# Kernel tuning notes

Hardware: AMD Instinct MI355X
Metric: run time of the kernel (lower is better)

Reference implementation:

```python
import jax, jax.numpy as jnp
import numpy as np

B = 4096        # batch size (graphs)
NPB = 64        # nodes per graph
G = 8           # max_groups; first G nodes of each graph are group super-nodes
D = 128         # node_dim
GD = 128        # global_dim
H = 64          # hidden_dim
NEG = jnp.float32(-1e9)


def setup_inputs() -> dict:
    key = jax.random.key(0)
    k = jax.random.split(key, 5)
    node_features = jax.random.normal(k[0], (B * NPB, D), dtype=jnp.float32)
    global_features = jax.random.normal(k[1], (B, GD), dtype=jnp.float32)
    # nodes sorted by graph: graph b owns rows [b*NPB, (b+1)*NPB)
    batch = jnp.repeat(jnp.arange(B, dtype=jnp.int64), NPB)
    local_id = jnp.tile(jnp.arange(NPB), B)
    group_mask_nodes = local_id < G            # exactly G group nodes per graph, in order
    dock_mask = jax.random.bernoulli(k[2], 0.7, (B, G, G))
    W1 = jax.random.normal(k[3], (GD + 2 * D, H), dtype=jnp.float32) * 0.05
    b1 = jnp.zeros((H,), dtype=jnp.float32)
    W2 = jax.random.normal(k[4], (H, 1), dtype=jnp.float32) * 0.05
    b2 = jnp.zeros((1,), dtype=jnp.float32)
    return {
        "node_features": node_features,
        "global_features": global_features,
        "group_mask_nodes": group_mask_nodes,
        "batch": batch,
        "dock_mask": dock_mask,
        "W1": W1, "b1": b1, "W2": W2, "b2": b2,
    }


def reference(node_features, global_features, group_mask_nodes, batch, dock_mask, W1, b1, W2, b2):
    bsz = global_features.shape[0]
    g = dock_mask.shape[1]
    d = node_features.shape[-1]
    # Gather group super-nodes. Rows are sorted by graph with exactly g group
    # nodes per graph, so a static-size nonzero reshapes to [B, G, D] preserving
    # the row order the torch loop relies on.
    idx = jnp.nonzero(group_mask_nodes, size=bsz * g)[0]
    group_nodes = node_features[idx].reshape(bsz, g, d)           # [B,G,D]
    # Build all (i,j) pair features: [global_b, g_i, g_j] -> [B,G,G,GD+2D]
    glob = jnp.broadcast_to(global_features[:, None, None, :], (bsz, g, g, global_features.shape[-1]))
    gi = jnp.broadcast_to(group_nodes[:, :, None, :], (bsz, g, g, d))
    gj = jnp.broadcast_to(group_nodes[:, None, :, :], (bsz, g, g, d))
    inp = jnp.concatenate([glob, gi, gj], axis=-1)
    # Tiny 2-layer MLP scorer, fully batched over all pairs.
    h = jax.nn.relu(jnp.einsum('bijf,fh->bijh', inp, W1) + b1)
    scores = jnp.einsum('bijh,ho->bijo', h, W2)[..., 0] + b2[0]   # [B,G,G]
    offdiag = ~jnp.eye(g, dtype=bool)
    logits = jnp.where(offdiag[None, :, :], scores, NEG)
    logits = jnp.where(dock_mask, logits, NEG)
    return logits.reshape(bsz, g * g)
```

## Files before the change

### kernel.cpp

```cpp
#include <hip/hip_runtime.h>
#include <hip/hip_bf16.h>

#define NEGV (-1e9f)

typedef __attribute__((ext_vector_type(8))) short short8;
typedef __attribute__((ext_vector_type(4))) float f32x4;

#define MFMA16(a, b, c) __builtin_amdgcn_mfma_f32_16x16x32_bf16(a, b, c, 0, 0, 0)

__device__ __forceinline__ unsigned short f2bf(float x) {
    union { __hip_bfloat16 h; unsigned short u; } c;
    c.h = __float2bfloat16(x);
    return c.u;
}

__device__ __forceinline__ short8 pack2(f32x4 a, f32x4 b) {
    short8 r;
    r[0] = (short)f2bf(a[0]); r[1] = (short)f2bf(a[1]);
    r[2] = (short)f2bf(a[2]); r[3] = (short)f2bf(a[3]);
    r[4] = (short)f2bf(b[0]); r[5] = (short)f2bf(b[1]);
    r[6] = (short)f2bf(b[2]); r[7] = (short)f2bf(b[3]);
    return r;
}

__device__ __forceinline__ void gather_mat(const float* __restrict__ Wp, int lg, short8* out4) {
    float tv[32];
#pragma unroll
    for (int x = 0; x < 32; ++x) {
        const int kt = x >> 3, i = x & 7;
        tv[x] = Wp[(kt * 32 + lg * 8 + i) * 64];
    }
#pragma unroll
    for (int kt = 0; kt < 4; ++kt) {
        short8 r;
#pragma unroll
        for (int i = 0; i < 8; ++i) r[i] = (short)f2bf(tv[kt * 8 + i]);
        out4[kt] = r;
    }
}

__global__ __launch_bounds__(256, 4) void dock_main(
    const float* __restrict__ nodes,
    const float* __restrict__ glob,
    const int*   __restrict__ dock,
    const float* __restrict__ W1,
    const float* __restrict__ b1,
    const float* __restrict__ b2,
    const float* __restrict__ W2,
    float* __restrict__ out)
{
    __shared__ __align__(16) unsigned char gA[32 * 256];
    __shared__ __align__(16) unsigned char gGl[16 * 256];
    __shared__ float sPQ[32][132];
    __shared__ float sA[4][68];

    const int t    = threadIdx.x;
    const int lane = t & 63;
    const int w    = __builtin_amdgcn_readfirstlane(t >> 6);
    const int b0   = blockIdx.x * 4;
    const int lr   = lane & 15, lg = lane >> 4;

    const int sr = t >> 3, sc0 = (t & 7) * 16;
    const f32x4* ns4 = (const f32x4*)(nodes + ((size_t)(b0 + (sr >> 3)) * 64 + (sr & 7)) * 128 + sc0);
    const f32x4 nf0 = ns4[0], nf1 = ns4[1], nf2 = ns4[2], nf3 = ns4[3];

    const int gr = t >> 4, gc0 = (t & 15) * 8;
    f32x4 gf0 = (f32x4)0.f, gf1 = (f32x4)0.f;
    if (gr < 4) {
        const f32x4* gs4 = (const f32x4*)(glob + (size_t)(b0 + gr) * 128 + gc0);
        gf0 = gs4[0]; gf1 = gs4[1];
    }
    const int idx   = (b0 + w) * 64 + lane;
    const int dmask = dock[idx];
    const float b1v = b1[w * 16 + lr];
    const float b2v = b2[0];

    const int n0 = w * 32 + lr;
    const int n1 = n0 + 16;
    const float* Wp0 = (n0 < 64) ? W1 + 128 * 64 + n0 : W1 + 256 * 64 + (n0 - 64);
    const float* Wp1 = (n1 < 64) ? W1 + 128 * 64 + n1 : W1 + 256 * 64 + (n1 - 64);
    const float* Wpg = W1 + (w * 16 + lr);

    short8 wf[12];
    gather_mat(Wp0, lg, wf);
    gather_mat(Wp1, lg, wf + 4);
    gather_mat(Wpg, lg, wf + 8);

    {
        const int u0 = sc0 >> 3;
        *(short8*)(gA + sr * 256 + ((u0 ^ (sr & 7)) << 4))       = pack2(nf0, nf1);
        *(short8*)(gA + sr * 256 + (((u0 + 1) ^ (sr & 7)) << 4)) = pack2(nf2, nf3);
        short8 gv = (short8)0;
        if (gr < 4) gv = pack2(gf0, gf1);
        *(short8*)(gGl + gr * 256 + (((gc0 >> 3) ^ (gr & 7)) << 4)) = gv;
    }
    __syncthreads();

    f32x4 acc00 = (f32x4)0.f, acc01 = (f32x4)0.f;
    f32x4 acc10 = (f32x4)0.f, acc11 = (f32x4)0.f;
    f32x4 accA  = (f32x4)0.f;
#pragma unroll
    for (int kt = 0; kt < 4; ++kt) {
        const int sw = ((kt * 4 + lg) ^ (lr & 7)) << 4;
        short8 aG0 = *(const short8*)(gA + lr * 256 + sw);
        short8 aG1 = *(const short8*)(gA + (16 + lr) * 256 + sw);
        short8 aGl = *(const short8*)(gGl + lr * 256 + sw);
        acc00 = MFMA16(aG0, wf[kt],     acc00);
        acc01 = MFMA16(aG0, wf[4 + kt], acc01);
        acc10 = MFMA16(aG1, wf[kt],     acc10);
        acc11 = MFMA16(aG1, wf[4 + kt], acc11);
        accA  = MFMA16(aGl, wf[8 + kt], accA);
    }

#pragma unroll
    for (int r = 0; r < 4; ++r) {
        sPQ[lg * 4 + r][w * 32 + lr]           = acc00[r];
        sPQ[lg * 4 + r][w * 32 + 16 + lr]      = acc01[r];
        sPQ[16 + lg * 4 + r][w * 32 + lr]      = acc10[r];
        sPQ[16 + lg * 4 + r][w * 32 + 16 + lr] = acc11[r];
    }
    if (lg == 0) {
#pragma unroll
        for (int r = 0; r < 4; ++r)
            sA[r][w * 16 + lr] = accA[r] + b1v;
    }
    __syncthreads();

    const int i = lane >> 3, j = lane & 7;
    const float* aRow = &sA[w][0];
    const float* pRow = &sPQ[w * 8 + i][0];
    const float* qRow = &sPQ[w * 8 + j][64];

    float s = 0.f;
#pragma unroll
    for (int kk = 0; kk < 64; kk += 4) {
        f32x4 a4 = *(const f32x4*)(aRow + kk);
        f32x4 p4 = *(const f32x4*)(pRow + kk);
        f32x4 q4 = *(const f32x4*)(qRow + kk);
        f32x4 w4 = *(const f32x4*)(W2 + kk);
#pragma unroll
        for (int u = 0; u < 4; ++u) {
            float h = a4[u] + p4[u] + q4[u];
            h = fmaxf(h, 0.f);
            s = fmaf(h, w4[u], s);
        }
    }
    s += b2v;

    out[idx] = ((i != j) && (dmask != 0)) ? s : NEGV;
}

extern "C" void kernel_launch(void* const* d_in, const int* in_sizes, int n_in,
                              void* d_out, int out_size, void* d_ws, size_t ws_size,
                              hipStream_t stream) {
    const float* nodes = (const float*)d_in[0];
    const float* glob  = (const float*)d_in[1];
    const int*   dock  = (const int*)d_in[4];
    const float* W1    = (const float*)d_in[5];
    const float* b1    = (const float*)d_in[6];
    const float* W2    = (const float*)d_in[7];
    const float* b2    = (const float*)d_in[8];
    float* out = (float*)d_out;

    const int B = in_sizes[1] / 128;
    dock_main<<<dim3(B / 4), dim3(256), 0, stream>>>(
        nodes, glob, dock, W1, b1, b2, W2, out);
}
```

Before: 15.17 us.

## Process two 4-graph tiles per block to amortize W1 fragment loads

Each block now handles 8 graphs as two sequential 4-graph tiles. The W1 bf16 fragments are gathered once and reused for both tiles, and the second tile's global loads are issued early to overlap with the first tile's work. The grid halves, occupancy hint drops to 2 blocks, and LDS doubles for the staging buffers. With only 512 blocks on a 256-CU part, fewer blocks risks weaker latency hiding.

```diff
diff --git a/kernel.cpp b/kernel.cpp
--- a/kernel.cpp
+++ b/kernel.cpp
@@ -7,6 +7,12 @@
 typedef __attribute__((ext_vector_type(4))) float f32x4;
 
 #define MFMA16(a, b, c) __builtin_amdgcn_mfma_f32_16x16x32_bf16(a, b, c, 0, 0, 0)
+
+#define BAR_LDS() do { \
+    asm volatile("s_waitcnt lgkmcnt(0)" ::: "memory"); \
+    __builtin_amdgcn_s_barrier(); \
+    asm volatile("" ::: "memory"); \
+} while (0)
 
 __device__ __forceinline__ unsigned short f2bf(float x) {
     union { __hip_bfloat16 h; unsigned short u; } c;
@@ -39,7 +45,66 @@
     }
 }
 
-__global__ __launch_bounds__(256, 4) void dock_main(
+struct Acc { f32x4 a00, a01, a10, a11, aA; };
+
+__device__ __forceinline__ Acc mfma_set(const unsigned char* gAb, const unsigned char* gGlb,
+                                        const short8* wf, int lr, int lg) {
+    Acc c;
+    c.a00 = (f32x4)0.f; c.a01 = (f32x4)0.f; c.a10 = (f32x4)0.f; c.a11 = (f32x4)0.f; c.aA = (f32x4)0.f;
+#pragma unroll
+    for (int kt = 0; kt < 4; ++kt) {
+        const int sw = ((kt * 4 + lg) ^ (lr & 7)) << 4;
+        short8 aG0 = *(const short8*)(gAb + lr * 256 + sw);
+        short8 aG1 = *(const short8*)(gAb + (16 + lr) * 256 + sw);
+        short8 aGl = *(const short8*)(gGlb + lr * 256 + sw);
+        c.a00 = MFMA16(aG0, wf[kt],     c.a00);
+        c.a01 = MFMA16(aG0, wf[4 + kt], c.a01);
+        c.a10 = MFMA16(aG1, wf[kt],     c.a10);
+        c.a11 = MFMA16(aG1, wf[4 + kt], c.a11);
+        c.aA  = MFMA16(aGl, wf[8 + kt], c.aA);
+    }
+    return c;
+}
+
+__device__ __forceinline__ void spill_set(const Acc& c, float (*sPQ)[132], float (*sA)[68],
+                                          int w, int lr, int lg, float b1v) {
+#pragma unroll
+    for (int r = 0; r < 4; ++r) {
+        sPQ[lg * 4 + r][w * 32 + lr]           = c.a00[r];
+        sPQ[lg * 4 + r][w * 32 + 16 + lr]      = c.a01[r];
+        sPQ[16 + lg * 4 + r][w * 32 + lr]      = c.a10[r];
+        sPQ[16 + lg * 4 + r][w * 32 + 16 + lr] = c.a11[r];
+    }
+    if (lg == 0) {
+#pragma unroll
+        for (int r = 0; r < 4; ++r) sA[r][w * 16 + lr] = c.aA[r] + b1v;
+    }
+}
+
+__device__ __forceinline__ float stage2(const float (*sPQ)[132], const float (*sA)[68],
+                                        const float* __restrict__ W2, int w, int lane) {
+    const int i = lane >> 3, j = lane & 7;
+    const float* aRow = &sA[w][0];
+    const float* pRow = &sPQ[w * 8 + i][0];
+    const float* qRow = &sPQ[w * 8 + j][64];
+    float s = 0.f;
+#pragma unroll
+    for (int kk = 0; kk < 64; kk += 4) {
+        f32x4 a4 = *(const f32x4*)(aRow + kk);
+        f32x4 p4 = *(const f32x4*)(pRow + kk);
+        f32x4 q4 = *(const f32x4*)(qRow + kk);
+        f32x4 w4 = *(const f32x4*)(W2 + kk);
+#pragma unroll
+        for (int u = 0; u < 4; ++u) {
+            float h = a4[u] + p4[u] + q4[u];
+            h = fmaxf(h, 0.f);
+            s = fmaf(h, w4[u], s);
+        }
+    }
+    return s;
+}
+
+__global__ __launch_bounds__(256, 2) void dock_main(
     const float* __restrict__ nodes,
     const float* __restrict__ glob,
     const int*   __restrict__ dock,
@@ -49,29 +114,30 @@
     const float* __restrict__ W2,
     float* __restrict__ out)
 {
-    __shared__ __align__(16) unsigned char gA[32 * 256];
-    __shared__ __align__(16) unsigned char gGl[16 * 256];
+    __shared__ __align__(16) unsigned char gA[2][8192];
+    __shared__ __align__(16) unsigned char gGl[2][4096];
     __shared__ float sPQ[32][132];
     __shared__ float sA[4][68];
 
     const int t    = threadIdx.x;
     const int lane = t & 63;
     const int w    = __builtin_amdgcn_readfirstlane(t >> 6);
-    const int b0   = blockIdx.x * 4;
     const int lr   = lane & 15, lg = lane >> 4;
+    const int b0   = blockIdx.x * 8;
 
     const int sr = t >> 3, sc0 = (t & 7) * 16;
-    const f32x4* ns4 = (const f32x4*)(nodes + ((size_t)(b0 + (sr >> 3)) * 64 + (sr & 7)) * 128 + sc0);
-    const f32x4 nf0 = ns4[0], nf1 = ns4[1], nf2 = ns4[2], nf3 = ns4[3];
-
     const int gr = t >> 4, gc0 = (t & 15) * 8;
-    f32x4 gf0 = (f32x4)0.f, gf1 = (f32x4)0.f;
+    const int u0 = sc0 >> 3;
+
+    const f32x4* ns0 = (const f32x4*)(nodes + ((size_t)(b0 + (sr >> 3)) * 64 + (sr & 7)) * 128 + sc0);
+    f32x4 n0a = ns0[0], n0b = ns0[1], n0c = ns0[2], n0d = ns0[3];
+    f32x4 g0a = (f32x4)0.f, g0b = (f32x4)0.f;
     if (gr < 4) {
-        const f32x4* gs4 = (const f32x4*)(glob + (size_t)(b0 + gr) * 128 + gc0);
-        gf0 = gs4[0]; gf1 = gs4[1];
-    }
-    const int idx   = (b0 + w) * 64 + lane;
-    const int dmask = dock[idx];
+        const f32x4* gs = (const f32x4*)(glob + (size_t)(b0 + gr) * 128 + gc0);
+        g0a = gs[0]; g0b = gs[1];
+    }
+    const int idx0 = (b0 + w) * 64 + lane;
+    const int dm0  = dock[idx0];
     const float b1v = b1[w * 16 + lr];
     const float b2v = b2[0];
 
@@ -80,74 +146,58 @@
     const float* Wp0 = (n0 < 64) ? W1 + 128 * 64 + n0 : W1 + 256 * 64 + (n0 - 64);
     const float* Wp1 = (n1 < 64) ? W1 + 128 * 64 + n1 : W1 + 256 * 64 + (n1 - 64);
     const float* Wpg = W1 + (w * 16 + lr);
-
     short8 wf[12];
     gather_mat(Wp0, lg, wf);
     gather_mat(Wp1, lg, wf + 4);
     gather_mat(Wpg, lg, wf + 8);
 
-    {
-        const int u0 = sc0 >> 3;
-        *(short8*)(gA + sr * 256 + ((u0 ^ (sr & 7)) << 4))       = pack2(nf0, nf1);
-        *(short8*)(gA + sr * 256 + (((u0 + 1) ^ (sr & 7)) << 4)) = pack2(nf2, nf3);
+    const f32x4* ns1 = (const f32x4*)(nodes + ((size_t)(b0 + 4 + (sr >> 3)) * 64 + (sr & 7)) * 128 + sc0);
+    f32x4 n1a = ns1[0], n1b = ns1[1], n1c = ns1[2], n1d = ns1[3];
+    f32x4 g1a = (f32x4)0.f, g1b = (f32x4)0.f;
+    if (gr < 4) {
+        const f32x4* gs = (const f32x4*)(glob + (size_t)(b0 + 4 + gr) * 128 + gc0);
+        g1a = gs[0]; g1b = gs[1];
+    }
+    const int idx1 = (b0 + 4 + w) * 64 + lane;
+    const int dm1  = dock[idx1];
+
+    *(short8*)(gA[0] + sr * 256 + ((u0 ^ (sr & 7)) << 4))       = pack2(n0a, n0b);
+    *(short8*)(gA[0] + sr * 256 + (((u0 + 1) ^ (sr & 7)) << 4)) = pack2(n0c, n0d);
+    {
         short8 gv = (short8)0;
-        if (gr < 4) gv = pack2(gf0, gf1);
-        *(short8*)(gGl + gr * 256 + (((gc0 >> 3) ^ (gr & 7)) << 4)) = gv;
-    }
-    __syncthreads();
-
-    f32x4 acc00 = (f32x4)0.f, acc01 = (f32x4)0.f;
-    f32x4 acc10 = (f32x4)0.f, acc11 = (f32x4)0.f;
-    f32x4 accA  = (f32x4)0.f;
-#pragma unroll
-    for (int kt = 0; kt < 4; ++kt) {
-        const int sw = ((kt * 4 + lg) ^ (lr & 7)) << 4;
-        short8 aG0 = *(const short8*)(gA + lr * 256 + sw);
-        short8 aG1 = *(const short8*)(gA + (16 + lr) * 256 + sw);
-        short8 aGl = *(const short8*)(gGl + lr * 256 + sw);
-        acc00 = MFMA16(aG0, wf[kt],     acc00);
-        acc01 = MFMA16(aG0, wf[4 + kt], acc01);
-        acc10 = MFMA16(aG1, wf[kt],     acc10);
-        acc11 = MFMA16(aG1, wf[4 + kt], acc11);
-        accA  = MFMA16(aGl, wf[8 + kt], accA);
-    }
-
-#pragma unroll
-    for (int r = 0; r < 4; ++r) {
-        sPQ[lg * 4 + r][w * 32 + lr]           = acc00[r];
-        sPQ[lg * 4 + r][w * 32 + 16 + lr]      = acc01[r];
-        sPQ[16 + lg * 4 + r][w * 32 + lr]      = acc10[r];
-        sPQ[16 + lg * 4 + r][w * 32 + 16 + lr] = acc11[r];
-    }
-    if (lg == 0) {
-#pragma unroll
-        for (int r = 0; r < 4; ++r)
-            sA[r][w * 16 + lr] = accA[r] + b1v;
-    }
-    __syncthreads();
-
-    const int i = lane >> 3, j = lane & 7;
-    const float* aRow = &sA[w][0];
-    const float* pRow = &sPQ[w * 8 + i][0];
-    const float* qRow = &sPQ[w * 8 + j][64];
-
-    float s = 0.f;
-#pragma unroll
-    for (int kk = 0; kk < 64; kk += 4) {
-        f32x4 a4 = *(const f32x4*)(aRow + kk);
-        f32x4 p4 = *(const f32x4*)(pRow + kk);
-        f32x4 q4 = *(const f32x4*)(qRow + kk);
-        f32x4 w4 = *(const f32x4*)(W2 + kk);
-#pragma unroll
-        for (int u = 0; u < 4; ++u) {
-            float h = a4[u] + p4[u] + q4[u];
-            h = fmaxf(h, 0.f);
-            s = fmaf(h, w4[u], s);
-        }
-    }
-    s += b2v;
-
-    out[idx] = ((i != j) && (dmask != 0)) ? s : NEGV;
+        if (gr < 4) gv = pack2(g0a, g0b);
+        *(short8*)(gGl[0] + gr * 256 + (((gc0 >> 3) ^ (gr & 7)) << 4)) = gv;
+    }
+    BAR_LDS();
+
+    Acc c0 = mfma_set(gA[0], gGl[0], wf, lr, lg);
+    spill_set(c0, sPQ, sA, w, lr, lg, b1v);
+    BAR_LDS();
+
+    *(short8*)(gA[1] + sr * 256 + ((u0 ^ (sr & 7)) << 4))       = pack2(n1a, n1b);
+    *(short8*)(gA[1] + sr * 256 + (((u0 + 1) ^ (sr & 7)) << 4)) = pack2(n1c, n1d);
+    {
+        short8 gv = (short8)0;
+        if (gr < 4) gv = pack2(g1a, g1b);
+        *(short8*)(gGl[1] + gr * 256 + (((gc0 >> 3) ^ (gr & 7)) << 4)) = gv;
+    }
+
+    {
+        const int i = lane >> 3, j = lane & 7;
+        float s = stage2(sPQ, sA, W2, w, lane) + b2v;
+        out[idx0] = ((i != j) && (dm0 != 0)) ? s : NEGV;
+    }
+    BAR_LDS();
+
+    Acc c1 = mfma_set(gA[1], gGl[1], wf, lr, lg);
+    spill_set(c1, sPQ, sA, w, lr, lg, b1v);
+    BAR_LDS();
+
+    {
+        const int i = lane >> 3, j = lane & 7;
+        float s = stage2(sPQ, sA, W2, w, lane) + b2v;
+        out[idx1] = ((i != j) && (dm1 != 0)) ? s : NEGV;
+    }
 }
 
 extern "C" void kernel_launch(void* const* d_in, const int* in_sizes, int n_in,
@@ -163,6 +213,6 @@
     float* out = (float*)d_out;
 
     const int B = in_sizes[1] / 128;
-    dock_main<<<dim3(B / 4), dim3(256), 0, stream>>>(
+    dock_main<<<dim3(B / 8), dim3(256), 0, stream>>>(
         nodes, glob, dock, W1, b1, b2, W2, out);
 }
```

After: 14.49 us (median of 2 runs). 1.05x faster.

## Split per-block work into two half-batches to overlap global loads with MFMA

Applied to the files above, without the earlier changes.

The block's four graphs are processed as two stages of two graphs each. The second stage's node and global rows are loaded from global memory while the first stage converts, stores to LDS and runs its MFMAs, so some of that latency is hidden. Global-feature rows now share the node tile buffer, and the global MFMA reads only two real rows instead of padding to sixteen. The cost is an extra barrier, more live registers, double-buffered LDS, and a per-stage MFMA count that fills less of the unit.

```diff
diff --git a/kernel.cpp b/kernel.cpp
--- a/kernel.cpp
+++ b/kernel.cpp
@@ -7,6 +7,12 @@
 typedef __attribute__((ext_vector_type(4))) float f32x4;
 
 #define MFMA16(a, b, c) __builtin_amdgcn_mfma_f32_16x16x32_bf16(a, b, c, 0, 0, 0)
+
+#define BAR_LDS() do { \
+    asm volatile("s_waitcnt lgkmcnt(0)" ::: "memory"); \
+    __builtin_amdgcn_s_barrier(); \
+    asm volatile("" ::: "memory"); \
+} while (0)
 
 __device__ __forceinline__ unsigned short f2bf(float x) {
     union { __hip_bfloat16 h; unsigned short u; } c;
@@ -49,29 +55,37 @@
     const float* __restrict__ W2,
     float* __restrict__ out)
 {
-    __shared__ __align__(16) unsigned char gA[32 * 256];
-    __shared__ __align__(16) unsigned char gGl[16 * 256];
-    __shared__ float sPQ[32][132];
-    __shared__ float sA[4][68];
+    __shared__ __align__(16) unsigned char gS[2][18 * 256];
+    __shared__ float sPQ[2][16][132];
+    __shared__ float sA[2][2][68];
 
     const int t    = threadIdx.x;
     const int lane = t & 63;
     const int w    = __builtin_amdgcn_readfirstlane(t >> 6);
+    const int lr   = lane & 15, lg = lane >> 4;
     const int b0   = blockIdx.x * 4;
-    const int lr   = lane & 15, lg = lane >> 4;
-
-    const int sr = t >> 3, sc0 = (t & 7) * 16;
-    const f32x4* ns4 = (const f32x4*)(nodes + ((size_t)(b0 + (sr >> 3)) * 64 + (sr & 7)) * 128 + sc0);
-    const f32x4 nf0 = ns4[0], nf1 = ns4[1], nf2 = ns4[2], nf3 = ns4[3];
-
-    const int gr = t >> 4, gc0 = (t & 15) * 8;
-    f32x4 gf0 = (f32x4)0.f, gf1 = (f32x4)0.f;
-    if (gr < 4) {
-        const f32x4* gs4 = (const f32x4*)(glob + (size_t)(b0 + gr) * 128 + gc0);
-        gf0 = gs4[0]; gf1 = gs4[1];
-    }
-    const int idx   = (b0 + w) * 64 + lane;
-    const int dmask = dock[idx];
+
+    const int R = t >> 3, c = t & 7;
+    const bool active = (t < 144);
+    const float* src0 = nodes;
+    const float* src1 = nodes;
+    if (active) {
+        if (R < 16) {
+            src0 = nodes + ((size_t)(b0 + (R >> 3)) * 64 + (R & 7)) * 128 + c * 16;
+            src1 = nodes + ((size_t)(b0 + 2 + (R >> 3)) * 64 + (R & 7)) * 128 + c * 16;
+        } else {
+            src0 = glob + (size_t)(b0 + (R - 16)) * 128 + c * 16;
+            src1 = glob + (size_t)(b0 + 2 + (R - 16)) * 128 + c * 16;
+        }
+    }
+
+    f32x4 L0[4];
+    if (active) {
+#pragma unroll
+        for (int x = 0; x < 4; ++x) L0[x] = ((const f32x4*)src0)[x];
+    }
+    const int idx = (b0 + w) * 64 + lane;
+    const int dm  = dock[idx];
     const float b1v = b1[w * 16 + lr];
     const float b2v = b2[0];
 
@@ -80,74 +94,100 @@
     const float* Wp0 = (n0 < 64) ? W1 + 128 * 64 + n0 : W1 + 256 * 64 + (n0 - 64);
     const float* Wp1 = (n1 < 64) ? W1 + 128 * 64 + n1 : W1 + 256 * 64 + (n1 - 64);
     const float* Wpg = W1 + (w * 16 + lr);
-
     short8 wf[12];
     gather_mat(Wp0, lg, wf);
     gather_mat(Wp1, lg, wf + 4);
     gather_mat(Wpg, lg, wf + 8);
 
+    if (active) {
+        const int u0 = c * 2;
+        *(short8*)(gS[0] + R * 256 + ((u0 ^ (R & 7)) << 4))       = pack2(L0[0], L0[1]);
+        *(short8*)(gS[0] + R * 256 + (((u0 + 1) ^ (R & 7)) << 4)) = pack2(L0[2], L0[3]);
+    }
+
+    f32x4 L1[4];
+    if (active) {
+#pragma unroll
+        for (int x = 0; x < 4; ++x) L1[x] = ((const f32x4*)src1)[x];
+    }
+    BAR_LDS();
+
     {
-        const int u0 = sc0 >> 3;
-        *(short8*)(gA + sr * 256 + ((u0 ^ (sr & 7)) << 4))       = pack2(nf0, nf1);
-        *(short8*)(gA + sr * 256 + (((u0 + 1) ^ (sr & 7)) << 4)) = pack2(nf2, nf3);
-        short8 gv = (short8)0;
-        if (gr < 4) gv = pack2(gf0, gf1);
-        *(short8*)(gGl + gr * 256 + (((gc0 >> 3) ^ (gr & 7)) << 4)) = gv;
-    }
-    __syncthreads();
-
-    f32x4 acc00 = (f32x4)0.f, acc01 = (f32x4)0.f;
-    f32x4 acc10 = (f32x4)0.f, acc11 = (f32x4)0.f;
-    f32x4 accA  = (f32x4)0.f;
-#pragma unroll
-    for (int kt = 0; kt < 4; ++kt) {
-        const int sw = ((kt * 4 + lg) ^ (lr & 7)) << 4;
-        short8 aG0 = *(const short8*)(gA + lr * 256 + sw);
-        short8 aG1 = *(const short8*)(gA + (16 + lr) * 256 + sw);
-        short8 aGl = *(const short8*)(gGl + lr * 256 + sw);
-        acc00 = MFMA16(aG0, wf[kt],     acc00);
-        acc01 = MFMA16(aG0, wf[4 + kt], acc01);
-        acc10 = MFMA16(aG1, wf[kt],     acc10);
-        acc11 = MFMA16(aG1, wf[4 + kt], acc11);
-        accA  = MFMA16(aGl, wf[8 + kt], accA);
-    }
-
-#pragma unroll
-    for (int r = 0; r < 4; ++r) {
-        sPQ[lg * 4 + r][w * 32 + lr]           = acc00[r];
-        sPQ[lg * 4 + r][w * 32 + 16 + lr]      = acc01[r];
-        sPQ[16 + lg * 4 + r][w * 32 + lr]      = acc10[r];
-        sPQ[16 + lg * 4 + r][w * 32 + 16 + lr] = acc11[r];
-    }
-    if (lg == 0) {
-#pragma unroll
-        for (int r = 0; r < 4; ++r)
-            sA[r][w * 16 + lr] = accA[r] + b1v;
-    }
-    __syncthreads();
-
-    const int i = lane >> 3, j = lane & 7;
-    const float* aRow = &sA[w][0];
-    const float* pRow = &sPQ[w * 8 + i][0];
-    const float* qRow = &sPQ[w * 8 + j][64];
-
-    float s = 0.f;
-#pragma unroll
-    for (int kk = 0; kk < 64; kk += 4) {
-        f32x4 a4 = *(const f32x4*)(aRow + kk);
-        f32x4 p4 = *(const f32x4*)(pRow + kk);
-        f32x4 q4 = *(const f32x4*)(qRow + kk);
-        f32x4 w4 = *(const f32x4*)(W2 + kk);
-#pragma unroll
-        for (int u = 0; u < 4; ++u) {
-            float h = a4[u] + p4[u] + q4[u];
-            h = fmaxf(h, 0.f);
-            s = fmaf(h, w4[u], s);
-        }
-    }
-    s += b2v;
-
-    out[idx] = ((i != j) && (dmask != 0)) ? s : NEGV;
+        f32x4 a0 = (f32x4)0.f, a1 = (f32x4)0.f, aA = (f32x4)0.f;
+#pragma unroll
+        for (int kt = 0; kt < 4; ++kt) {
+            const int sw  = ((kt * 4 + lg) ^ (lr & 7)) << 4;
+            const int swg = ((kt * 4 + lg) ^ (lr & 1)) << 4;
+            short8 aG  = *(const short8*)(gS[0] + lr * 256 + sw);
+            short8 aGl = *(const short8*)(gS[0] + (16 + (lr & 1)) * 256 + swg);
+            a0 = MFMA16(aG,  wf[kt],     a0);
+            a1 = MFMA16(aG,  wf[4 + kt], a1);
+            aA = MFMA16(aGl, wf[8 + kt], aA);
+        }
+#pragma unroll
+        for (int r = 0; r < 4; ++r) {
+            sPQ[0][lg * 4 + r][w * 32 + lr]      = a0[r];
+            sPQ[0][lg * 4 + r][w * 32 + 16 + lr] = a1[r];
+        }
+        if (lg == 0) {
+#pragma unroll
+            for (int r = 0; r < 2; ++r) sA[0][r][w * 16 + lr] = aA[r] + b1v;
+        }
+    }
+    if (active) {
+        const int u0 = c * 2;
+        *(short8*)(gS[1] + R * 256 + ((u0 ^ (R & 7)) << 4))       = pack2(L1[0], L1[1]);
+        *(short8*)(gS[1] + R * 256 + (((u0 + 1) ^ (R & 7)) << 4)) = pack2(L1[2], L1[3]);
+    }
+    BAR_LDS();
+
+    {
+        f32x4 a0 = (f32x4)0.f, a1 = (f32x4)0.f, aA = (f32x4)0.f;
+#pragma unroll
+        for (int kt = 0; kt < 4; ++kt) {
+            const int sw  = ((kt * 4 + lg) ^ (lr & 7)) << 4;
+            const int swg = ((kt * 4 + lg) ^ (lr & 1)) << 4;
+            short8 aG  = *(const short8*)(gS[1] + lr * 256 + sw);
+            short8 aGl = *(const short8*)(gS[1] + (16 + (lr & 1)) * 256 + swg);
+            a0 = MFMA16(aG,  wf[kt],     a0);
+            a1 = MFMA16(aG,  wf[4 + kt], a1);
+            aA = MFMA16(aGl, wf[8 + kt], aA);
+        }
+#pragma unroll
+        for (int r = 0; r < 4; ++r) {
+            sPQ[1][lg * 4 + r][w * 32 + lr]      = a0[r];
+            sPQ[1][lg * 4 + r][w * 32 + 16 + lr] = a1[r];
+        }
+        if (lg == 0) {
+#pragma unroll
+            for (int r = 0; r < 2; ++r) sA[1][r][w * 16 + lr] = aA[r] + b1v;
+        }
+    }
+    BAR_LDS();
+
+    {
+        const int s = w >> 1, g = w & 1;
+        const int i = lane >> 3, j = lane & 7;
+        const float* aRow = &sA[s][g][0];
+        const float* pRow = &sPQ[s][g * 8 + i][0];
+        const float* qRow = &sPQ[s][g * 8 + j][64];
+        float sc = 0.f;
+#pragma unroll
+        for (int kk = 0; kk < 64; kk += 4) {
+            f32x4 a4 = *(const f32x4*)(aRow + kk);
+            f32x4 p4 = *(const f32x4*)(pRow + kk);
+            f32x4 q4 = *(const f32x4*)(qRow + kk);
+            f32x4 w4 = *(const f32x4*)(W2 + kk);
+#pragma unroll
+            for (int u = 0; u < 4; ++u) {
+                float h = a4[u] + p4[u] + q4[u];
+                h = fmaxf(h, 0.f);
+                sc = fmaf(h, w4[u], sc);
+            }
+        }
+        sc += b2v;
+        out[idx] = ((i != j) && (dm != 0)) ? sc : NEGV;
+    }
 }
 
 extern "C" void kernel_launch(void* const* d_in, const int* in_sizes, int n_in,
```

Measured after the change: 19.74 us. +30.1%, slower.
